# Kernel tuning notes

Hardware: AMD Instinct MI355X
Metric: run time of the kernel (lower is better)

The kernel has to match this reference:

```python
import jax, jax.numpy as jnp
import numpy as np

B, S = 32, 2048
DIM_ACTION = 32
DIM_STRUCT = 64
HIDDEN = 128  # mlp_hidden_dim default = dim_action * 4
EPS = 1e-12   # F.normalize eps


def l2norm(t):
    n = jnp.linalg.norm(t, axis=-1, keepdims=True)
    return t / jnp.maximum(n, EPS)


def setup_inputs() -> dict:
    key = jax.random.key(0)
    ks = jax.random.split(key, 9)
    sd = lambda fan_in: 1.0 / np.sqrt(fan_in)
    inp = {
        "actions": jax.random.normal(ks[0], (B, S, DIM_ACTION), dtype=jnp.float32),
        # MLP: dim_action -> hidden -> hidden -> dim_structure^2 (depth=2 hidden relu layers)
        "w0": jax.random.uniform(ks[1], (DIM_ACTION, HIDDEN), jnp.float32, -sd(DIM_ACTION), sd(DIM_ACTION)),
        "b0": jnp.zeros((HIDDEN,), jnp.float32),
        "w1": jax.random.uniform(ks[2], (HIDDEN, HIDDEN), jnp.float32, -sd(HIDDEN), sd(HIDDEN)),
        "b1": jnp.zeros((HIDDEN,), jnp.float32),
        "w2": jax.random.uniform(ks[3], (HIDDEN, DIM_STRUCT * DIM_STRUCT), jnp.float32, -sd(HIDDEN), sd(HIDDEN)),
        "b2": jnp.zeros((DIM_STRUCT * DIM_STRUCT,), jnp.float32),
        # RNN init hidden parameter [1, dim_structure], ~N(0, 0.01)
        "init_hidden": jax.random.normal(ks[4], (1, DIM_STRUCT), dtype=jnp.float32) * 0.01,
    }
    return inp


def reference(actions, w0, b0, w1, b1, w2, b2, init_hidden):
    # MLP to transitions: [B, S, d*d]
    h = jax.nn.relu(jnp.einsum("bsa,ah->bsh", actions, w0) + b0)
    h = jax.nn.relu(jnp.einsum("bsh,hk->bsk", h, w1) + b1)
    t = jnp.einsum("bsh,ho->bso", h, w2) + b2
    transitions = t.reshape(B, S, DIM_STRUCT, DIM_STRUCT)  # [B, S, i, j]

    # RNN: hidden_{t+1} = l2norm(relu(hidden_t @ T_t)), scanned over seq
    hidden0 = jnp.broadcast_to(l2norm(init_hidden), (B, DIM_STRUCT))

    def step(hidden, trans):  # trans: [B, i, j]
        hidden = jnp.einsum("bi,bij->bj", hidden, trans)
        hidden = l2norm(jax.nn.relu(hidden))
        return hidden, hidden

    trans_seq = jnp.swapaxes(transitions, 0, 1)  # [S, B, i, j]
    _, hiddens = jax.lax.scan(step, hidden0, trans_seq)  # [S, B, d]
    return jnp.swapaxes(hiddens, 0, 1)  # [B, S, d]
```

## Files before the change

kernel.cpp:

```cpp
#include <hip/hip_runtime.h>

#define B_ 32
#define S_ 2048
#define DA 32
#define DH 128
#define DS 64
#define DS2 4096
#define TKK 16

template <int CTRL>
__device__ __forceinline__ float dpp_add(float x) {
  int t = __builtin_amdgcn_update_dpp(0, __float_as_int(x), CTRL, 0xF, 0xF, true);
  return x + __int_as_float(t);
}
__device__ __forceinline__ float row_sum16(float x) {
  x = dpp_add<0xB1>(x);
  x = dpp_add<0x4E>(x);
  x = dpp_add<0x141>(x);
  x = dpp_add<0x140>(x);
  return x;
}

__device__ __forceinline__ void gl2lds16(const float* g, float* l) {
  __builtin_amdgcn_global_load_lds(
      (const __attribute__((address_space(1))) void*)g,
      (__attribute__((address_space(3))) void*)l, 16, 0, 0);
}

struct SharedGemm {
  float As[2][TKK][128];
  float Bs[2][TKK][128];
};
struct SharedMlp {
  float a_t[DA][64];
  float w0_l[DA][DH];
  float h0t[DH][64];
};
union SharedU {
  SharedGemm g;
  SharedMlp m;
};

__device__ __forceinline__ void mlp_tile(
    const float* __restrict__ actions, const float* __restrict__ w0,
    const float* __restrict__ b0, const float* __restrict__ w1,
    const float* __restrict__ b1, float* __restrict__ h1t,
    int s_base, int M, int m0, SharedMlp& sm, int tid)
{
#pragma unroll
  for (int q = 0; q < 2; ++q) {
    int g = tid + 256 * q;
    int tok = g >> 3, kq = g & 7;
    int tl = m0 + tok;
    int b = tl & 31, s = s_base + (tl >> 5);
    float4 v = *(const float4*)(actions + ((size_t)b * S_ + s) * DA + 4 * kq);
    sm.a_t[4 * kq + 0][tok] = v.x; sm.a_t[4 * kq + 1][tok] = v.y;
    sm.a_t[4 * kq + 2][tok] = v.z; sm.a_t[4 * kq + 3][tok] = v.w;
  }
#pragma unroll
  for (int q = 0; q < 4; ++q) {
    int g = tid + 256 * q;
    ((float4*)&sm.w0_l[0][0])[g] = ((const float4*)w0)[g];
  }
  __syncthreads();

  const int tm = tid & 15;
  const int tn = tid >> 4;

  float acc[4][8];
#pragma unroll
  for (int mi = 0; mi < 4; ++mi)
#pragma unroll
    for (int ni = 0; ni < 8; ++ni) acc[mi][ni] = 0.f;

#pragma unroll 4
  for (int k = 0; k < DA; ++k) {
    float4 a4 = *(const float4*)&sm.a_t[k][4 * tm];
    float4 wa = *(const float4*)&sm.w0_l[k][8 * tn];
    float4 wb = *(const float4*)&sm.w0_l[k][8 * tn + 4];
    float av[4] = {a4.x, a4.y, a4.z, a4.w};
    float wv[8] = {wa.x, wa.y, wa.z, wa.w, wb.x, wb.y, wb.z, wb.w};
#pragma unroll
    for (int mi = 0; mi < 4; ++mi)
#pragma unroll
      for (int ni = 0; ni < 8; ++ni) acc[mi][ni] += av[mi] * wv[ni];
  }
  {
    float4 ba = *(const float4*)(b0 + 8 * tn);
    float4 bb = *(const float4*)(b0 + 8 * tn + 4);
    float bv[8] = {ba.x, ba.y, ba.z, ba.w, bb.x, bb.y, bb.z, bb.w};
#pragma unroll
    for (int mi = 0; mi < 4; ++mi)
#pragma unroll
      for (int ni = 0; ni < 8; ++ni)
        sm.h0t[8 * tn + ni][4 * tm + mi] = fmaxf(acc[mi][ni] + bv[ni], 0.f);
  }
  __syncthreads();

  float acc1[4][8];
#pragma unroll
  for (int mi = 0; mi < 4; ++mi)
#pragma unroll
    for (int ni = 0; ni < 8; ++ni) acc1[mi][ni] = 0.f;

#pragma unroll 4
  for (int k = 0; k < DH; ++k) {
    float4 h4 = *(const float4*)&sm.h0t[k][4 * tm];
    float4 wa = *(const float4*)(w1 + (size_t)k * DH + 8 * tn);
    float4 wb = *(const float4*)(w1 + (size_t)k * DH + 8 * tn + 4);
    float av[4] = {h4.x, h4.y, h4.z, h4.w};
    float wv[8] = {wa.x, wa.y, wa.z, wa.w, wb.x, wb.y, wb.z, wb.w};
#pragma unroll
    for (int mi = 0; mi < 4; ++mi)
#pragma unroll
      for (int ni = 0; ni < 8; ++ni) acc1[mi][ni] += av[mi] * wv[ni];
  }
  {
    float4 ba = *(const float4*)(b1 + 8 * tn);
    float4 bb = *(const float4*)(b1 + 8 * tn + 4);
    float bv[8] = {ba.x, ba.y, ba.z, ba.w, bb.x, bb.y, bb.z, bb.w};
#pragma unroll
    for (int ni = 0; ni < 8; ++ni) {
      float4 o;
      o.x = fmaxf(acc1[0][ni] + bv[ni], 0.f);
      o.y = fmaxf(acc1[1][ni] + bv[ni], 0.f);
      o.z = fmaxf(acc1[2][ni] + bv[ni], 0.f);
      o.w = fmaxf(acc1[3][ni] + bv[ni], 0.f);
      *(float4*)(h1t + (size_t)(8 * tn + ni) * M + m0 + 4 * tm) = o;
    }
  }
}

__device__ __forceinline__ void trans_tile(
    const float* __restrict__ h1t, const float* __restrict__ w2,
    const float* __restrict__ b2, float* __restrict__ trans,
    int M, int n0, int m0, SharedGemm& sg, int tid)
{
  const int w  = tid >> 6;
  const int lw = tid & 63;

  auto aload = [&](int t, int buf) {
#pragma unroll
    for (int ii = 0; ii < 2; ++ii) {
      const int i = 2 * w + ii;
      const int kr = 2 * i + (lw >> 5);
      const int c4 = 4 * (lw & 31);
      gl2lds16(h1t + (size_t)(t * TKK + kr) * M + m0 + c4, &sg.As[buf][2 * i][0]);
      gl2lds16(w2 + (size_t)(t * TKK + kr) * DS2 + n0 + c4, &sg.Bs[buf][2 * i][0]);
    }
  };

  aload(0, 0);

  const int mg = tid >> 4;
  const int ng = tid & 15;
  float acc[8][8];
#pragma unroll
  for (int mi = 0; mi < 8; ++mi)
#pragma unroll
    for (int ni = 0; ni < 8; ++ni) acc[mi][ni] = 0.f;

  int buf = 0;
  for (int t = 0; t < DH / TKK; ++t) {
    __syncthreads();
    if (t < DH / TKK - 1) aload(t + 1, buf ^ 1);
#pragma unroll
    for (int k = 0; k < TKK; ++k) {
      float4 a0 = *(const float4*)&sg.As[buf][k][8 * mg];
      float4 a1 = *(const float4*)&sg.As[buf][k][8 * mg + 4];
      float av[8] = {a0.x, a0.y, a0.z, a0.w, a1.x, a1.y, a1.z, a1.w};
      float4 b0v = *(const float4*)&sg.Bs[buf][k][4 * ng];
      float4 b1v = *(const float4*)&sg.Bs[buf][k][64 + 4 * ng];
      float bv[8] = {b0v.x, b0v.y, b0v.z, b0v.w, b1v.x, b1v.y, b1v.z, b1v.w};
#pragma unroll
      for (int mi = 0; mi < 8; ++mi)
#pragma unroll
        for (int ni = 0; ni < 8; ++ni) acc[mi][ni] += av[mi] * bv[ni];
    }
    buf ^= 1;
  }

  float4 bb0 = *(const float4*)(b2 + n0 + 4 * ng);
  float4 bb1 = *(const float4*)(b2 + n0 + 64 + 4 * ng);
  float bv[8] = {bb0.x, bb0.y, bb0.z, bb0.w, bb1.x, bb1.y, bb1.z, bb1.w};
#pragma unroll
  for (int mi = 0; mi < 8; ++mi) {
    float* dst = trans + (size_t)(m0 + 8 * mg + mi) * DS2 + n0;
#pragma unroll
    for (int q = 0; q < 2; ++q) {
      float4 o;
      o.x = acc[mi][4 * q + 0] + bv[4 * q + 0];
      o.y = acc[mi][4 * q + 1] + bv[4 * q + 1];
      o.z = acc[mi][4 * q + 2] + bv[4 * q + 2];
      o.w = acc[mi][4 * q + 3] + bv[4 * q + 3];
      *(float4*)(dst + 64 * q + 4 * ng) = o;
    }
  }
}

__global__ __launch_bounds__(256) void k_mlp01(
    const float* __restrict__ actions, const float* __restrict__ w0,
    const float* __restrict__ b0, const float* __restrict__ w1,
    const float* __restrict__ b1, float* __restrict__ h1t,
    int s_base, int M)
{
  __shared__ SharedMlp sm;
  mlp_tile(actions, w0, b0, w1, b1, h1t, s_base, M, blockIdx.x * 64, sm,
           threadIdx.x);
}

__global__ __launch_bounds__(256, 2) void k_comb(
    const float* __restrict__ actions, const float* __restrict__ w0,
    const float* __restrict__ b0, const float* __restrict__ w1,
    const float* __restrict__ b1, const float* __restrict__ w2,
    const float* __restrict__ b2, const float* __restrict__ init_hidden,
    float* __restrict__ trans0, float* __restrict__ trans1,
    float* __restrict__ h1t0, float* __restrict__ h1t1,
    float* __restrict__ hstate, float* __restrict__ out,
    int c, int SC, int nch)
{
  __shared__ SharedU sh;
  const int tid = threadIdx.x;
  const int M = SC * 32;

  if (blockIdx.x >= 32) {
    const int bi = blockIdx.x - 32;
    if (c < nch) {
      const float* h1t = (c & 1) ? h1t1 : h1t0;
      float* trans = (c & 1) ? trans1 : trans0;
      const int NJ = (M / 128) * (DS2 / 128);
      for (int j = bi; j < NJ; j += 448) {
        const int mt = j >> 5, nt = j & 31;
        trans_tile(h1t, w2, b2, trans, M, nt * 128, mt * 128, sh.g, tid);
        __syncthreads();
      }
      if (c + 1 < nch) {
        __syncthreads();
        float* h1n = ((c + 1) & 1) ? h1t1 : h1t0;
        for (int j = bi; j < M / 64; j += 448) {
          mlp_tile(actions, w0, b0, w1, b1, h1n, (c + 1) * SC, M, j * 64,
                   sh.m, tid);
          __syncthreads();
        }
      }
    }
    return;
  }

  if (c == 0) return;
  if (tid >= 64) return;
  const int cc = c - 1;
  const float* trans = (cc & 1) ? trans1 : trans0;
  const int s_base = cc * SC;
  const int lane = tid;
  const int b = blockIdx.x;

  const int d = lane >> 4;
  const int cq = lane & 15;
  const bool d1 = (d & 1), d2 = (d & 2);
  const int pb = lane & 48;

  float4 hq;
  if (cc == 0) {
    hq = *(const float4*)(init_hidden + 4 * cq);
    float ss0 = row_sum16(hq.x * hq.x + hq.y * hq.y + hq.z * hq.z + hq.w * hq.w);
    float iv0 = 1.0f / fmaxf(sqrtf(ss0), 1e-12f);
    hq.x *= iv0; hq.y *= iv0; hq.z *= iv0; hq.w *= iv0;
  } else {
    hq = *(const float4*)(hstate + b * DS + 4 * cq);
  }
  float inv_prev = 1.0f;

  float* outp = out + ((size_t)b * S_ + s_base) * DS + 4 * cq;
  const float* g0 = trans + (size_t)b * DS2 + 4 * lane;
  const size_t sstride = (size_t)32 * DS2;

  auto step_fn = [&](const float4 (&T)[16], int s) {
    float hsel = d2 ? (d1 ? hq.w : hq.z) : (d1 ? hq.y : hq.x);
    float ax = 0.f, ay = 0.f, az = 0.f, aw = 0.f;
#pragma unroll
    for (int q = 0; q < 16; ++q) {
      float hb = __shfl(hsel, pb + q, 64);
      ax += hb * T[q].x; ay += hb * T[q].y;
      az += hb * T[q].z; aw += hb * T[q].w;
    }
    ax += __shfl_xor(ax, 16, 64); ax += __shfl_xor(ax, 32, 64);
    ay += __shfl_xor(ay, 16, 64); ay += __shfl_xor(ay, 32, 64);
    az += __shfl_xor(az, 16, 64); az += __shfl_xor(az, 32, 64);
    aw += __shfl_xor(aw, 16, 64); aw += __shfl_xor(aw, 32, 64);
    hq.x = fmaxf(ax * inv_prev, 0.f);
    hq.y = fmaxf(ay * inv_prev, 0.f);
    hq.z = fmaxf(az * inv_prev, 0.f);
    hq.w = fmaxf(aw * inv_prev, 0.f);
    float ss = row_sum16(hq.x * hq.x + hq.y * hq.y + hq.z * hq.z + hq.w * hq.w);
    float inv = 1.0f / fmaxf(sqrtf(ss), 1e-12f);
    if (d == 0) {
      float4 o;
      o.x = hq.x * inv; o.y = hq.y * inv; o.z = hq.z * inv; o.w = hq.w * inv;
      *(float4*)(outp + (size_t)s * DS) = o;
    }
    inv_prev = inv;
  };

  float4 A[16], Bv[16];
#pragma unroll
  for (int q = 0; q < 16; ++q) A[q] = *(const float4*)(g0 + q * 256);

  for (int s = 0; s < SC; s += 2) {
    const float* g1 = g0 + (size_t)(s + 1) * sstride;
#pragma unroll
    for (int q = 0; q < 16; ++q) Bv[q] = *(const float4*)(g1 + q * 256);
    step_fn(A, s);
    if (s + 2 < SC) {
      const float* g2 = g0 + (size_t)(s + 2) * sstride;
#pragma unroll
      for (int q = 0; q < 16; ++q) A[q] = *(const float4*)(g2 + q * 256);
    }
    step_fn(Bv, s + 1);
  }

  if (d == 0) {
    float4 o;
    o.x = hq.x * inv_prev; o.y = hq.y * inv_prev;
    o.z = hq.z * inv_prev; o.w = hq.w * inv_prev;
    *(float4*)(hstate + b * DS + 4 * cq) = o;
  }
}

extern "C" void kernel_launch(void* const* d_in, const int* in_sizes, int n_in,
                              void* d_out, int out_size, void* d_ws, size_t ws_size,
                              hipStream_t stream) {
  const float* actions     = (const float*)d_in[0];
  const float* w0          = (const float*)d_in[1];
  const float* b0          = (const float*)d_in[2];
  const float* w1          = (const float*)d_in[3];
  const float* b1          = (const float*)d_in[4];
  const float* w2          = (const float*)d_in[5];
  const float* b2          = (const float*)d_in[6];
  const float* init_hidden = (const float*)d_in[7];
  float* out = (float*)d_out;

  int SC = 2048;
  while (SC > 4) {
    size_t need = 2 * ((size_t)SC * 32 * DS2 * 4 + (size_t)SC * 32 * DH * 4)
                + (size_t)B_ * DS * 4;
    if (need <= ws_size) break;
    SC >>= 1;
  }
  float* trans0 = (float*)d_ws;
  float* trans1 = trans0 + (size_t)SC * 32 * DS2;
  float* h1t0   = trans1 + (size_t)SC * 32 * DS2;
  float* h1t1   = h1t0 + (size_t)SC * 32 * DH;
  float* hstate = h1t1 + (size_t)SC * 32 * DH;

  const int M = SC * 32;
  const int nch = S_ / SC;

  hipLaunchKernelGGL(k_mlp01, dim3(M / 64), dim3(256), 0, stream,
                     actions, w0, b0, w1, b1, h1t0, 0, M);
  for (int c = 0; c <= nch; ++c) {
    hipLaunchKernelGGL(k_comb, dim3(480), dim3(256), 0, stream,
                       actions, w0, b0, w1, b1, w2, b2, init_hidden,
                       trans0, trans1, h1t0, h1t1, hstate, out, c, SC, nch);
  }
}
```

Before: 1.727 ms.

## Compute transition GEMM with split-fp16 MFMA and whole-K LDS tiles

```diff
diff --git a/kernel.cpp b/kernel.cpp
--- a/kernel.cpp
+++ b/kernel.cpp
@@ -6,7 +6,9 @@
 #define DH 128
 #define DS 64
 #define DS2 4096
-#define TKK 16
+
+typedef _Float16 half8 __attribute__((ext_vector_type(8)));
+typedef float f32x4 __attribute__((ext_vector_type(4)));
 
 template <int CTRL>
 __device__ __forceinline__ float dpp_add(float x) {
@@ -21,15 +23,17 @@
   return x;
 }
 
-__device__ __forceinline__ void gl2lds16(const float* g, float* l) {
+__device__ __forceinline__ void gl2lds16(const void* g, void* l) {
   __builtin_amdgcn_global_load_lds(
       (const __attribute__((address_space(1))) void*)g,
       (__attribute__((address_space(3))) void*)l, 16, 0, 0);
 }
 
 struct SharedGemm {
-  float As[2][TKK][128];
-  float Bs[2][TKK][128];
+  _Float16 Ah[128 * 128];
+  _Float16 Al[128 * 128];
+  _Float16 Bh[128 * 128];
+  _Float16 Bl[128 * 128];
 };
 struct SharedMlp {
   float a_t[DA][64];
@@ -41,11 +45,27 @@
   SharedMlp m;
 };
 
+__global__ __launch_bounds__(256) void k_split(
+    const float* __restrict__ w2, _Float16* __restrict__ w2h,
+    _Float16* __restrict__ w2l)
+{
+  for (int e = blockIdx.x * 256 + threadIdx.x; e < DH * DS2;
+       e += gridDim.x * 256) {
+    int n = e >> 7, k = e & 127;
+    float v = w2[(size_t)k * DS2 + n];
+    _Float16 hi = (_Float16)v;
+    _Float16 lo = (_Float16)((v - (float)hi) * 2048.0f);
+    int kk = k ^ ((n & 7) << 3);
+    w2h[(size_t)n * DH + kk] = hi;
+    w2l[(size_t)n * DH + kk] = lo;
+  }
+}
+
 __device__ __forceinline__ void mlp_tile(
     const float* __restrict__ actions, const float* __restrict__ w0,
     const float* __restrict__ b0, const float* __restrict__ w1,
-    const float* __restrict__ b1, float* __restrict__ h1t,
-    int s_base, int M, int m0, SharedMlp& sm, int tid)
+    const float* __restrict__ b1, _Float16* __restrict__ h1h,
+    _Float16* __restrict__ h1l, int s_base, int m0, SharedMlp& sm, int tid)
 {
 #pragma unroll
   for (int q = 0; q < 2; ++q) {
@@ -120,80 +140,120 @@
     float4 bb = *(const float4*)(b1 + 8 * tn + 4);
     float bv[8] = {ba.x, ba.y, ba.z, ba.w, bb.x, bb.y, bb.z, bb.w};
 #pragma unroll
-    for (int ni = 0; ni < 8; ++ni) {
-      float4 o;
-      o.x = fmaxf(acc1[0][ni] + bv[ni], 0.f);
-      o.y = fmaxf(acc1[1][ni] + bv[ni], 0.f);
-      o.z = fmaxf(acc1[2][ni] + bv[ni], 0.f);
-      o.w = fmaxf(acc1[3][ni] + bv[ni], 0.f);
-      *(float4*)(h1t + (size_t)(8 * tn + ni) * M + m0 + 4 * tm) = o;
-    }
-  }
-}
-
-__device__ __forceinline__ void trans_tile(
-    const float* __restrict__ h1t, const float* __restrict__ w2,
+    for (int mi = 0; mi < 4; ++mi) {
+      const int m = m0 + 4 * tm + mi;
+      half8 hv, lv;
+#pragma unroll
+      for (int ni = 0; ni < 8; ++ni) {
+        float h = fmaxf(acc1[mi][ni] + bv[ni], 0.f);
+        _Float16 hi = (_Float16)h;
+        hv[ni] = hi;
+        lv[ni] = (_Float16)((h - (float)hi) * 2048.0f);
+      }
+      const int off = m * DH + ((8 * tn) ^ ((m & 7) << 3));
+      *(half8*)(h1h + off) = hv;
+      *(half8*)(h1l + off) = lv;
+    }
+  }
+}
+
+__device__ __forceinline__ void trans_loop(
+    const _Float16* __restrict__ h1h, const _Float16* __restrict__ h1l,
+    const _Float16* __restrict__ w2h, const _Float16* __restrict__ w2l,
     const float* __restrict__ b2, float* __restrict__ trans,
-    int M, int n0, int m0, SharedGemm& sg, int tid)
+    int MT, int x, SharedGemm& sg, int tid)
 {
   const int w  = tid >> 6;
   const int lw = tid & 63;
-
-  auto aload = [&](int t, int buf) {
-#pragma unroll
-    for (int ii = 0; ii < 2; ++ii) {
-      const int i = 2 * w + ii;
-      const int kr = 2 * i + (lw >> 5);
-      const int c4 = 4 * (lw & 31);
-      gl2lds16(h1t + (size_t)(t * TKK + kr) * M + m0 + c4, &sg.As[buf][2 * i][0]);
-      gl2lds16(w2 + (size_t)(t * TKK + kr) * DS2 + n0 + c4, &sg.Bs[buf][2 * i][0]);
-    }
+  const int strip = x / 7;
+  const int idx   = x % 7;
+  const int n0 = strip * 128;
+
+  auto stage32k = [&](const _Float16* src, _Float16* dst) {
+    const _Float16* s = src + w * 4096 + lw * 8;
+    _Float16* d = dst + w * 4096;
+#pragma unroll
+    for (int i = 0; i < 8; ++i)
+      gl2lds16(s + i * 512, d + i * 512);
   };
 
-  aload(0, 0);
-
-  const int mg = tid >> 4;
-  const int ng = tid & 15;
-  float acc[8][8];
-#pragma unroll
-  for (int mi = 0; mi < 8; ++mi)
-#pragma unroll
-    for (int ni = 0; ni < 8; ++ni) acc[mi][ni] = 0.f;
-
-  int buf = 0;
-  for (int t = 0; t < DH / TKK; ++t) {
+  stage32k(w2h + (size_t)n0 * DH, sg.Bh);
+  stage32k(w2l + (size_t)n0 * DH, sg.Bl);
+
+  const int fr = lw & 15;
+  const int kg = lw >> 4;
+  const int wr = w >> 1, wc = w & 1;
+
+  float b2v[4];
+#pragma unroll
+  for (int fn = 0; fn < 4; ++fn)
+    b2v[fn] = b2[n0 + wc * 64 + fn * 16 + fr];
+
+  const f32x4 fz = {0.f, 0.f, 0.f, 0.f};
+
+  for (int mt = idx; mt < MT; mt += 7) {
+    const int m0 = mt * 128;
+    stage32k(h1h + (size_t)m0 * DH, sg.Ah);
+    stage32k(h1l + (size_t)m0 * DH, sg.Al);
+    asm volatile("s_waitcnt vmcnt(0)" ::: "memory");
     __syncthreads();
-    if (t < DH / TKK - 1) aload(t + 1, buf ^ 1);
-#pragma unroll
-    for (int k = 0; k < TKK; ++k) {
-      float4 a0 = *(const float4*)&sg.As[buf][k][8 * mg];
-      float4 a1 = *(const float4*)&sg.As[buf][k][8 * mg + 4];
-      float av[8] = {a0.x, a0.y, a0.z, a0.w, a1.x, a1.y, a1.z, a1.w};
-      float4 b0v = *(const float4*)&sg.Bs[buf][k][4 * ng];
-      float4 b1v = *(const float4*)&sg.Bs[buf][k][64 + 4 * ng];
-      float bv[8] = {b0v.x, b0v.y, b0v.z, b0v.w, b1v.x, b1v.y, b1v.z, b1v.w};
-#pragma unroll
-      for (int mi = 0; mi < 8; ++mi)
-#pragma unroll
-        for (int ni = 0; ni < 8; ++ni) acc[mi][ni] += av[mi] * bv[ni];
-    }
-    buf ^= 1;
-  }
-
-  float4 bb0 = *(const float4*)(b2 + n0 + 4 * ng);
-  float4 bb1 = *(const float4*)(b2 + n0 + 64 + 4 * ng);
-  float bv[8] = {bb0.x, bb0.y, bb0.z, bb0.w, bb1.x, bb1.y, bb1.z, bb1.w};
-#pragma unroll
-  for (int mi = 0; mi < 8; ++mi) {
-    float* dst = trans + (size_t)(m0 + 8 * mg + mi) * DS2 + n0;
-#pragma unroll
-    for (int q = 0; q < 2; ++q) {
-      float4 o;
-      o.x = acc[mi][4 * q + 0] + bv[4 * q + 0];
-      o.y = acc[mi][4 * q + 1] + bv[4 * q + 1];
-      o.z = acc[mi][4 * q + 2] + bv[4 * q + 2];
-      o.w = acc[mi][4 * q + 3] + bv[4 * q + 3];
-      *(float4*)(dst + 64 * q + 4 * ng) = o;
+
+    f32x4 ahh[4][4], axx[4][4], all_[4][4];
+#pragma unroll
+    for (int fm = 0; fm < 4; ++fm)
+#pragma unroll
+      for (int fn = 0; fn < 4; ++fn) {
+        ahh[fm][fn] = fz;
+        axx[fm][fn] = fz;
+        all_[fm][fn] = fz;
+      }
+
+#pragma unroll
+    for (int kc = 0; kc < 4; ++kc) {
+      const int k0 = kc * 32 + kg * 8;
+      half8 bh[4], bl[4];
+#pragma unroll
+      for (int fn = 0; fn < 4; ++fn) {
+        const int n = wc * 64 + fn * 16 + fr;
+        const int off = n * DH + (k0 ^ ((n & 7) << 3));
+        bh[fn] = *(const half8*)&sg.Bh[off];
+        bl[fn] = *(const half8*)&sg.Bl[off];
+      }
+#pragma unroll
+      for (int fm = 0; fm < 4; ++fm) {
+        const int m = wr * 64 + fm * 16 + fr;
+        const int off = m * DH + (k0 ^ ((m & 7) << 3));
+        half8 ah = *(const half8*)&sg.Ah[off];
+        half8 al = *(const half8*)&sg.Al[off];
+#pragma unroll
+        for (int fn = 0; fn < 4; ++fn) {
+          ahh[fm][fn] = __builtin_amdgcn_mfma_f32_16x16x32_f16(
+              ah, bh[fn], ahh[fm][fn], 0, 0, 0);
+          axx[fm][fn] = __builtin_amdgcn_mfma_f32_16x16x32_f16(
+              ah, bl[fn], axx[fm][fn], 0, 0, 0);
+          axx[fm][fn] = __builtin_amdgcn_mfma_f32_16x16x32_f16(
+              al, bh[fn], axx[fm][fn], 0, 0, 0);
+          all_[fm][fn] = __builtin_amdgcn_mfma_f32_16x16x32_f16(
+              al, bl[fn], all_[fm][fn], 0, 0, 0);
+        }
+      }
+    }
+    __syncthreads();
+
+#pragma unroll
+    for (int fm = 0; fm < 4; ++fm) {
+#pragma unroll
+      for (int fn = 0; fn < 4; ++fn) {
+        const int col = n0 + wc * 64 + fn * 16 + fr;
+        float* dst = trans +
+            (size_t)(m0 + wr * 64 + fm * 16 + kg * 4) * DS2 + col;
+#pragma unroll
+        for (int r = 0; r < 4; ++r) {
+          float v = ahh[fm][fn][r] + axx[fm][fn][r] * (1.0f / 2048.0f) +
+                    all_[fm][fn][r] * (1.0f / 4194304.0f) + b2v[fn];
+          dst[(size_t)r * DS2] = v;
+        }
+      }
     }
   }
 }
@@ -201,21 +261,23 @@
 __global__ __launch_bounds__(256) void k_mlp01(
     const float* __restrict__ actions, const float* __restrict__ w0,
     const float* __restrict__ b0, const float* __restrict__ w1,
-    const float* __restrict__ b1, float* __restrict__ h1t,
-    int s_base, int M)
+    const float* __restrict__ b1, _Float16* __restrict__ h1h,
+    _Float16* __restrict__ h1l, int s_base)
 {
   __shared__ SharedMlp sm;
-  mlp_tile(actions, w0, b0, w1, b1, h1t, s_base, M, blockIdx.x * 64, sm,
+  mlp_tile(actions, w0, b0, w1, b1, h1h, h1l, s_base, blockIdx.x * 64, sm,
            threadIdx.x);
 }
 
-__global__ __launch_bounds__(256, 2) void k_comb(
+__global__ __launch_bounds__(256, 1) void k_comb(
     const float* __restrict__ actions, const float* __restrict__ w0,
     const float* __restrict__ b0, const float* __restrict__ w1,
-    const float* __restrict__ b1, const float* __restrict__ w2,
-    const float* __restrict__ b2, const float* __restrict__ init_hidden,
+    const float* __restrict__ b1, const _Float16* __restrict__ w2h,
+    const _Float16* __restrict__ w2l, const float* __restrict__ b2,
+    const float* __restrict__ init_hidden,
     float* __restrict__ trans0, float* __restrict__ trans1,
-    float* __restrict__ h1t0, float* __restrict__ h1t1,
+    _Float16* __restrict__ h1h0, _Float16* __restrict__ h1l0,
+    _Float16* __restrict__ h1h1, _Float16* __restrict__ h1l1,
     float* __restrict__ hstate, float* __restrict__ out,
     int c, int SC, int nch)
 {
@@ -224,21 +286,18 @@
   const int M = SC * 32;
 
   if (blockIdx.x >= 32) {
-    const int bi = blockIdx.x - 32;
+    const int x = blockIdx.x - 32;
     if (c < nch) {
-      const float* h1t = (c & 1) ? h1t1 : h1t0;
+      const _Float16* h1h = (c & 1) ? h1h1 : h1h0;
+      const _Float16* h1l = (c & 1) ? h1l1 : h1l0;
       float* trans = (c & 1) ? trans1 : trans0;
-      const int NJ = (M / 128) * (DS2 / 128);
-      for (int j = bi; j < NJ; j += 448) {
-        const int mt = j >> 5, nt = j & 31;
-        trans_tile(h1t, w2, b2, trans, M, nt * 128, mt * 128, sh.g, tid);
-        __syncthreads();
-      }
+      trans_loop(h1h, h1l, w2h, w2l, b2, trans, M / 128, x, sh.g, tid);
       if (c + 1 < nch) {
         __syncthreads();
-        float* h1n = ((c + 1) & 1) ? h1t1 : h1t0;
-        for (int j = bi; j < M / 64; j += 448) {
-          mlp_tile(actions, w0, b0, w1, b1, h1n, (c + 1) * SC, M, j * 64,
+        _Float16* hh = ((c + 1) & 1) ? h1h1 : h1h0;
+        _Float16* hl = ((c + 1) & 1) ? h1l1 : h1l0;
+        for (int j = x; j < M / 64; j += 224) {
+          mlp_tile(actions, w0, b0, w1, b1, hh, hl, (c + 1) * SC, j * 64,
                    sh.m, tid);
           __syncthreads();
         }
@@ -342,25 +401,34 @@
 
   int SC = 2048;
   while (SC > 4) {
-    size_t need = 2 * ((size_t)SC * 32 * DS2 * 4 + (size_t)SC * 32 * DH * 4)
+    size_t need = 2 * (size_t)SC * 32 * DS2 * 4
+                + 4 * (size_t)SC * 32 * DH * 2
+                + 2 * (size_t)DH * DS2 * 2
                 + (size_t)B_ * DS * 4;
     if (need <= ws_size) break;
     SC >>= 1;
   }
-  float* trans0 = (float*)d_ws;
-  float* trans1 = trans0 + (size_t)SC * 32 * DS2;
-  float* h1t0   = trans1 + (size_t)SC * 32 * DS2;
-  float* h1t1   = h1t0 + (size_t)SC * 32 * DH;
-  float* hstate = h1t1 + (size_t)SC * 32 * DH;
+  char* p = (char*)d_ws;
+  float* trans0 = (float*)p;        p += (size_t)SC * 32 * DS2 * 4;
+  float* trans1 = (float*)p;        p += (size_t)SC * 32 * DS2 * 4;
+  _Float16* h1h0 = (_Float16*)p;    p += (size_t)SC * 32 * DH * 2;
+  _Float16* h1l0 = (_Float16*)p;    p += (size_t)SC * 32 * DH * 2;
+  _Float16* h1h1 = (_Float16*)p;    p += (size_t)SC * 32 * DH * 2;
+  _Float16* h1l1 = (_Float16*)p;    p += (size_t)SC * 32 * DH * 2;
+  _Float16* w2h  = (_Float16*)p;    p += (size_t)DH * DS2 * 2;
+  _Float16* w2l  = (_Float16*)p;    p += (size_t)DH * DS2 * 2;
+  float* hstate  = (float*)p;
 
   const int M = SC * 32;
   const int nch = S_ / SC;
 
+  hipLaunchKernelGGL(k_split, dim3(512), dim3(256), 0, stream, w2, w2h, w2l);
   hipLaunchKernelGGL(k_mlp01, dim3(M / 64), dim3(256), 0, stream,
-                     actions, w0, b0, w1, b1, h1t0, 0, M);
+                     actions, w0, b0, w1, b1, h1h0, h1l0, 0);
   for (int c = 0; c <= nch; ++c) {
-    hipLaunchKernelGGL(k_comb, dim3(480), dim3(256), 0, stream,
-                       actions, w0, b0, w1, b1, w2, b2, init_hidden,
-                       trans0, trans1, h1t0, h1t1, hstate, out, c, SC, nch);
-  }
-}
+    hipLaunchKernelGGL(k_comb, dim3(256), dim3(256), 0, stream,
+                       actions, w0, b0, w1, b1, w2h, w2l, b2, init_hidden,
+                       trans0, trans1, h1h0, h1l0, h1h1, h1l1, hstate, out,
+                       c, SC, nch);
+  }
+}
```

Measured after the change: 1.586 ms. 8.1% less time.
